# Kernel tuning notes

Hardware: AMD Instinct MI355X
Metric: run time of the kernel (lower is better)

The kernel has to match this reference:

```python
import jax, jax.numpy as jnp
import numpy as np
from jax.scipy.special import logsumexp

B, N, D = 8, 1500, 256
ITERS = 50


def _mlp(x, W1, b1, W2, b2, W3, b3):
    # DETR-style MLP: ReLU between layers, linear last
    h = jax.nn.relu(x @ W1 + b1)
    h = jax.nn.relu(h @ W2 + b2)
    return h @ W3 + b3


def _log_sinkhorn(Z, log_mu, log_nu, iters):
    # Z: [b, m+1, n+1]; loop-carried dual potentials u, v
    u0 = jnp.zeros_like(log_mu)
    v0 = jnp.zeros_like(log_nu)

    def step(carry, _):
        u, v = carry
        u = log_mu - logsumexp(Z + v[:, None, :], axis=2)
        v = log_nu - logsumexp(Z + u[:, :, None], axis=1)
        return (u, v), None

    (u, v), _ = jax.lax.scan(step, (u0, v0), None, length=iters)
    return Z + u[:, :, None] + v[:, None, :]


def _log_optimal_transport(scores, alpha, iters):
    b, m, n = scores.shape
    bins0 = jnp.broadcast_to(alpha, (b, m, 1))
    bins1 = jnp.broadcast_to(alpha, (b, 1, n))
    a = jnp.broadcast_to(alpha, (b, 1, 1))
    couplings = jnp.concatenate(
        [jnp.concatenate([scores, bins0], -1), jnp.concatenate([bins1, a], -1)], 1
    )  # [b, m+1, n+1]
    dt = scores.dtype
    norm = -jnp.log(jnp.asarray(m + n, dt))
    log_mu = jnp.concatenate([jnp.full((m,), norm, dt), jnp.log(jnp.asarray(n, dt))[None] + norm])
    log_nu = jnp.concatenate([jnp.full((n,), norm, dt), jnp.log(jnp.asarray(m, dt))[None] + norm])
    log_mu = jnp.broadcast_to(log_mu[None], (b, m + 1))
    log_nu = jnp.broadcast_to(log_nu[None], (b, n + 1))
    Z = _log_sinkhorn(couplings, log_mu, log_nu, iters)
    return Z - norm


def setup_inputs() -> dict:
    key = jax.random.key(0)
    k = jax.random.split(key, 6)
    s = 0.05
    return {
        "quer_feat": jax.random.normal(k[0], (B, N, D), jnp.float32),
        "pos_start": jax.random.normal(k[1], (B, N, D), jnp.float32),
        "pos_end": jax.random.normal(k[2], (B, N, D), jnp.float32),
        "W1": jax.random.normal(k[3], (2 * D, D), jnp.float32) * s,
        "b1": jnp.zeros((D,), jnp.float32),
        "W2": jax.random.normal(k[4], (D, D), jnp.float32) * s,
        "b2": jnp.zeros((D,), jnp.float32),
        "W3": jax.random.normal(k[5], (D, D), jnp.float32) * s,
        "b3": jnp.zeros((D,), jnp.float32),
        "bin_score": jnp.asarray(1.0, jnp.float32),
        "iters": ITERS,
    }


def reference(quer_feat, pos_start, pos_end, W1, b1, W2, b2, W3, b3, bin_score, iters):
    # forward_single with shared_projection + similarity_based + sinkhorn
    f1 = _mlp(jnp.concatenate([quer_feat, pos_end], -1), W1, b1, W2, b2, W3, b3)
    f2 = _mlp(jnp.concatenate([quer_feat, pos_start], -1), W1, b1, W2, b2, W3, b3)
    scores = jnp.einsum("bnc,bmc->bnm", f1, f2) / jnp.sqrt(jnp.asarray(D, f1.dtype))
    i = jnp.arange(scores.shape[1])
    scores = scores.at[:, i, i].set(-jnp.inf)  # no self-connection
    Z = _log_optimal_transport(scores, bin_score, iters)
    return jnp.exp(Z)
```

## Files before the change

kernel.cpp:

```cpp
#include <hip/hip_runtime.h>
#include <hip/hip_fp16.h>

#define BATCH 8
#define NPTS 1500
#define DIM 256
#define M1 1501
#define KH 1536
#define MROWS 24000
#define ITERS 50
#define MU_PT (1.0f / 3000.0f)
#define MU_BIN 0.5f

typedef _Float16 half8 __attribute__((ext_vector_type(8)));
typedef float f32x4 __attribute__((ext_vector_type(4)));

__device__ __forceinline__ float4 ld4(const float* p){ return *(const float4*)p; }

__global__ void prep_w_kernel(const float* __restrict__ W1, const float* __restrict__ W2,
                              const float* __restrict__ W3, __half* __restrict__ Wt1,
                              __half* __restrict__ Wt2, __half* __restrict__ Wt3)
{
  int gid = blockIdx.x * 256 + threadIdx.x;
  if (gid < 512 * 256) {
    int n = gid >> 9, k = gid & 511;
    Wt1[gid] = __float2half(W1[k * 256 + n]);
  } else if (gid < 512 * 256 + 256 * 256) {
    int g = gid - 512 * 256; int n = g >> 8, k = g & 255;
    Wt2[g] = __float2half(W2[k * 256 + n]);
  } else if (gid < 512 * 256 + 2 * 256 * 256) {
    int g = gid - 512 * 256 - 256 * 256; int n = g >> 8, k = g & 255;
    Wt3[g] = __float2half(W3[k * 256 + n]);
  }
}

template<int MODE>
__global__ __launch_bounds__(256) void mfma_gemm_kernel(
    const float* __restrict__ Aq, const float* __restrict__ Ap_end,
    const float* __restrict__ Ap_start, const __half* __restrict__ Ah,
    const __half* __restrict__ Bh, const float* __restrict__ bias,
    __half* __restrict__ out)
{
  const int K = (MODE == 0) ? 512 : 256;
  const int M = (MODE == 3) ? NPTS : MROWS;
  __shared__ _Float16 As[128][40];
  __shared__ _Float16 Bs[128][40];
  const int t = threadIdx.x;
  const int lane = t & 63;
  const int wave = t >> 6;
  const int quad = lane >> 4, l15 = lane & 15;
  const int wm = wave & 1, wn = wave >> 1;
  const int m0 = blockIdx.x * 128;
  const int n0 = blockIdx.y * 128;
  const int b  = (MODE == 3) ? blockIdx.z : 0;
  const __half* F1 = Ah + (size_t)b * NPTS * 256;
  const __half* F2 = Ah + (size_t)(12000 + b * NPTS) * 256;

  f32x4 acc[4][4];
#pragma unroll
  for (int i = 0; i < 4; ++i)
#pragma unroll
    for (int j = 0; j < 4; ++j) acc[i][j] = (f32x4){0.f, 0.f, 0.f, 0.f};

  const int sr = t >> 1;
  const int c0 = (t & 1) * 16;

  for (int kt = 0; kt < K; kt += 32) {
    {
      int grow = m0 + sr;
      if (MODE == 0) {
        union { half8 v[2]; _Float16 s[16]; } U;
        if (grow < M) {
          int col = kt + c0;
          int r12 = (grow < 12000) ? grow : grow - 12000;
          const float* src;
          if (col < 256) src = Aq + (size_t)r12 * 256 + col;
          else src = ((grow < 12000) ? Ap_end : Ap_start) + (size_t)r12 * 256 + (col - 256);
#pragma unroll
          for (int i = 0; i < 4; ++i) {
            float4 w = ld4(src + 4 * i);
            U.s[4*i+0] = (_Float16)w.x; U.s[4*i+1] = (_Float16)w.y;
            U.s[4*i+2] = (_Float16)w.z; U.s[4*i+3] = (_Float16)w.w;
          }
        } else {
#pragma unroll
          for (int i = 0; i < 16; ++i) U.s[i] = (_Float16)0.f;
        }
        *(half8*)&As[sr][c0]     = U.v[0];
        *(half8*)&As[sr][c0 + 8] = U.v[1];
      } else {
        const __half* src = ((MODE == 3) ? F1 : Ah) + (size_t)grow * 256 + kt + c0;
        uint4 u0 = make_uint4(0,0,0,0), u1 = make_uint4(0,0,0,0);
        if (grow < M) { u0 = *(const uint4*)src; u1 = *(const uint4*)(src + 8); }
        *(uint4*)&As[sr][c0]     = u0;
        *(uint4*)&As[sr][c0 + 8] = u1;
      }
    }
    {
      int n = n0 + sr;
      uint4 u0 = make_uint4(0,0,0,0), u1 = make_uint4(0,0,0,0);
      if (MODE == 3) {
        if (n < NPTS) {
          const __half* src = F2 + (size_t)n * 256 + kt + c0;
          u0 = *(const uint4*)src; u1 = *(const uint4*)(src + 8);
        }
      } else {
        const __half* src = Bh + (size_t)n * K + kt + c0;
        u0 = *(const uint4*)src; u1 = *(const uint4*)(src + 8);
      }
      *(uint4*)&Bs[sr][c0]     = u0;
      *(uint4*)&Bs[sr][c0 + 8] = u1;
    }
    __syncthreads();
    half8 af[4], bf[4];
#pragma unroll
    for (int sm = 0; sm < 4; ++sm)
      af[sm] = *(half8*)&As[wm * 64 + sm * 16 + l15][quad * 8];
#pragma unroll
    for (int sn = 0; sn < 4; ++sn)
      bf[sn] = *(half8*)&Bs[wn * 64 + sn * 16 + l15][quad * 8];
#pragma unroll
    for (int sm = 0; sm < 4; ++sm)
#pragma unroll
      for (int sn = 0; sn < 4; ++sn)
        acc[sm][sn] = __builtin_amdgcn_mfma_f32_16x16x32_f16(af[sm], bf[sn], acc[sm][sn], 0, 0, 0);
    __syncthreads();
  }

  if (MODE == 3) {
    __half* Kb = out + (size_t)b * M1 * KH;
#pragma unroll
    for (int sm = 0; sm < 4; ++sm) {
      int rbase = m0 + wm * 64 + sm * 16 + quad * 4;
#pragma unroll
      for (int reg = 0; reg < 4; ++reg) {
        int gi = rbase + reg;
        if (gi < NPTS) {
#pragma unroll
          for (int sn = 0; sn < 4; ++sn) {
            int gj = n0 + wn * 64 + sn * 16 + l15;
            float v = acc[sm][sn][reg] * 0.0625f;
            float kv = (gj < NPTS && gj != gi) ? __expf(v) : 0.f;
            Kb[(size_t)gi * KH + gj] = __float2half(kv);
          }
        }
      }
    }
  } else {
    float bv[4];
#pragma unroll
    for (int sn = 0; sn < 4; ++sn) bv[sn] = bias[n0 + wn * 64 + sn * 16 + l15];
#pragma unroll
    for (int sm = 0; sm < 4; ++sm) {
      int rbase = m0 + wm * 64 + sm * 16 + quad * 4;
#pragma unroll
      for (int reg = 0; reg < 4; ++reg) {
        int gr = rbase + reg;
        if (gr < MROWS) {
#pragma unroll
          for (int sn = 0; sn < 4; ++sn) {
            int col = n0 + wn * 64 + sn * 16 + l15;
            float v = acc[sm][sn][reg] + bv[sn];
            if (MODE != 2) v = fmaxf(v, 0.f);
            out[(size_t)gr * 256 + col] = __float2half(v);
          }
        }
      }
    }
  }
}

__global__ void bins_kernel(__half* __restrict__ Kh, const float* __restrict__ palpha,
                            float* __restrict__ csum0)
{
  int gid = blockIdx.x * 256 + threadIdx.x;
  if (gid >= BATCH * KH) return;
  int b = gid / KH, x = gid % KH;
  __half He = __float2half(expf(palpha[0]));
  __half* Kb = Kh + (size_t)b * M1 * KH;
  csum0[gid] = 0.f;
  if (x < M1) {
    Kb[(size_t)NPTS * KH + x] = He;
    Kb[(size_t)x * KH + NPTS] = He;
  } else {
    Kb[(size_t)NPTS * KH + x] = __float2half(0.f);
  }
}

__global__ __launch_bounds__(256) void sink_iter_kernel(
    const __half* __restrict__ Kh,
    const float* __restrict__ csum_prev,
    float* __restrict__ csum_cur,
    float* __restrict__ csum_zero,
    float* __restrict__ eu, int first)
{
  const int t = threadIdx.x;
  const int wave = t >> 6, lane = t & 63;
  const int bb = blockIdx.x & 7;
  const int rb = blockIdx.x >> 3;
  const int wv = (rb << 2) | wave;
  const __half* Kb = Kh + (size_t)bb * M1 * KH;
  float* eub = eu + bb * KH;

  __shared__ __align__(16) float evs[KH];
  __shared__ __align__(16) float wpart[4][KH];

  if (rb == 0) {
    for (int j = t; j < KH; j += 256) csum_zero[bb * KH + j] = 0.f;
  }
  if (first) {
    for (int j = t; j < KH; j += 256) evs[j] = (j < M1) ? 1.0f : 0.f;
  } else {
    for (int j = t; j < KH; j += 256) {
      float nu = (j < NPTS) ? MU_PT : ((j == NPTS) ? MU_BIN : 0.f);
      evs[j] = (j < M1) ? (nu / csum_prev[bb * KH + j]) : 0.f;
    }
  }
  __syncthreads();

  float acc[24];
#pragma unroll
  for (int k = 0; k < 24; ++k) acc[k] = 0.f;

  for (int i = wv; i < M1; i += 256) {
    const __half* row = Kb + (size_t)i * KH;
    float r[24];
    float dot = 0.f;
#pragma unroll
    for (int k = 0; k < 3; ++k) {
      int c = lane + (k << 6);
      union { uint4 u; __half2 h[4]; } U;
      U.u = *(const uint4*)(row + (c << 3));
#pragma unroll
      for (int m = 0; m < 4; ++m) {
        float2 f = __half22float2(U.h[m]);
        r[k * 8 + 2 * m]     = f.x;
        r[k * 8 + 2 * m + 1] = f.y;
      }
      float4 e0 = *(const float4*)&evs[(c << 3)];
      float4 e1 = *(const float4*)&evs[(c << 3) + 4];
      dot += r[k*8+0]*e0.x + r[k*8+1]*e0.y + r[k*8+2]*e0.z + r[k*8+3]*e0.w
           + r[k*8+4]*e1.x + r[k*8+5]*e1.y + r[k*8+6]*e1.z + r[k*8+7]*e1.w;
    }
#pragma unroll
    for (int off = 32; off > 0; off >>= 1) dot += __shfl_xor(dot, off);
    float mu = (i < NPTS) ? MU_PT : MU_BIN;
    float euv = mu / dot;
    if (lane == 0) eub[i] = euv;
#pragma unroll
    for (int k = 0; k < 24; ++k) acc[k] += r[k] * euv;
  }

#pragma unroll
  for (int k = 0; k < 3; ++k) {
    int c = lane + (k << 6);
    float4 a0 = make_float4(acc[k*8+0], acc[k*8+1], acc[k*8+2], acc[k*8+3]);
    float4 a1 = make_float4(acc[k*8+4], acc[k*8+5], acc[k*8+6], acc[k*8+7]);
    *(float4*)&wpart[wave][(c << 3)]     = a0;
    *(float4*)&wpart[wave][(c << 3) + 4] = a1;
  }
  __syncthreads();
  for (int j = t; j < M1; j += 256) {
    float s = wpart[0][j] + wpart[1][j] + wpart[2][j] + wpart[3][j];
    atomicAdd(&csum_cur[bb * KH + j], s);
  }
}

__global__ void final_ev_kernel(const float* __restrict__ csum,
                                float* __restrict__ ev)
{
  int j = blockIdx.x * 256 + threadIdx.x;
  int bb = blockIdx.y;
  if (j >= M1) return;
  float nu = (j < NPTS) ? MU_PT : MU_BIN;
  ev[bb * KH + j] = nu / csum[bb * KH + j];
}

__global__ __launch_bounds__(256) void finalize_kernel(
    const __half* __restrict__ Kh, const float* __restrict__ eu,
    const float* __restrict__ ev, float* __restrict__ out)
{
  int rowid = blockIdx.x;
  int b = rowid / M1, i = rowid % M1;
  const __half* krow = Kh + ((size_t)b * M1 + i) * KH;
  const float* evb = ev + b * KH;
  float* orow = out + (size_t)rowid * M1;
  float scale = eu[b * KH + i] * 3000.0f;
  for (int j = threadIdx.x; j < M1; j += 256)
    orow[j] = __half2float(krow[j]) * evb[j] * scale;
}

extern "C" void kernel_launch(void* const* d_in, const int* in_sizes, int n_in,
                              void* d_out, int out_size, void* d_ws, size_t ws_size,
                              hipStream_t stream)
{
  const float* quer      = (const float*)d_in[0];
  const float* pos_start = (const float*)d_in[1];
  const float* pos_end   = (const float*)d_in[2];
  const float* W1 = (const float*)d_in[3];
  const float* b1 = (const float*)d_in[4];
  const float* W2 = (const float*)d_in[5];
  const float* b2 = (const float*)d_in[6];
  const float* W3 = (const float*)d_in[7];
  const float* b3 = (const float*)d_in[8];
  const float* alpha = (const float*)d_in[9];

  char* ws = (char*)d_ws;
  size_t off = 0;
  auto carve = [&](size_t bytes) -> void* {
    void* p = ws + off;
    off += (bytes + 1023) & ~(size_t)1023;
    return p;
  };
  __half* Ha  = (__half*)carve((size_t)MROWS * 256 * 2);
  __half* Hb  = (__half*)carve((size_t)MROWS * 256 * 2);
  __half* Kh  = (__half*)carve((size_t)BATCH * M1 * KH * 2);
  __half* Wt1 = (__half*)carve((size_t)256 * 512 * 2);
  __half* Wt2 = (__half*)carve((size_t)256 * 256 * 2);
  __half* Wt3 = (__half*)carve((size_t)256 * 256 * 2);
  float* csum[3];
  for (int c = 0; c < 3; ++c) csum[c] = (float*)carve((size_t)BATCH * KH * 4);
  float* eu = (float*)carve((size_t)BATCH * KH * 4);
  float* ev = (float*)carve((size_t)BATCH * KH * 4);
  (void)ws_size; (void)in_sizes; (void)n_in; (void)out_size;

  dim3 blk(256);
  prep_w_kernel<<<dim3(1024), blk, 0, stream>>>(W1, W2, W3, Wt1, Wt2, Wt3);
  mfma_gemm_kernel<0><<<dim3(188, 2), blk, 0, stream>>>(quer, pos_end, pos_start, nullptr, Wt1, b1, Ha);
  mfma_gemm_kernel<1><<<dim3(188, 2), blk, 0, stream>>>(nullptr, nullptr, nullptr, Ha, Wt2, b2, Hb);
  mfma_gemm_kernel<2><<<dim3(188, 2), blk, 0, stream>>>(nullptr, nullptr, nullptr, Hb, Wt3, b3, Ha);
  mfma_gemm_kernel<3><<<dim3(12, 12, 8), blk, 0, stream>>>(nullptr, nullptr, nullptr, Ha, nullptr, nullptr, Kh);
  bins_kernel<<<dim3((BATCH * KH + 255) / 256), blk, 0, stream>>>(Kh, alpha, csum[0]);
  for (int it = 0; it < ITERS; ++it) {
    float* prev = csum[(it + 2) % 3];
    float* cur  = csum[it % 3];
    float* znxt = csum[(it + 1) % 3];
    sink_iter_kernel<<<dim3(512), blk, 0, stream>>>(Kh, prev, cur, znxt, eu, it == 0 ? 1 : 0);
  }
  final_ev_kernel<<<dim3(6, 8), blk, 0, stream>>>(csum[(ITERS - 1) % 3], ev);
  finalize_kernel<<<dim3(BATCH * M1), blk, 0, stream>>>(Kh, eu, ev, (float*)d_out);
}
```

Measured before the change: 788.1 us.

## Fuse Sinkhorn iterations into one persistent kernel with register-resident K

Replaces the 50 per-iteration launches with a single persistent kernel of 512 blocks. Each block keeps its rows of the half-precision kernel matrix in registers, so K is loaded from global memory once instead of on every iteration. Blocks synchronize per batch through a global atomic counter barrier, and the finalize step is folded into the same kernel. The risks are a deadlock if all 512 blocks are not co-resident (launch bounds ask for 2 blocks per CU), heavy register pressure, and LDS atomic contention.

```diff
diff --git a/kernel.cpp b/kernel.cpp
--- a/kernel.cpp
+++ b/kernel.cpp
@@ -10,6 +10,7 @@
 #define ITERS 50
 #define MU_PT (1.0f / 3000.0f)
 #define MU_BIN 0.5f
+#define NBB 64
 
 typedef _Float16 half8 __attribute__((ext_vector_type(8)));
 typedef float f32x4 __attribute__((ext_vector_type(4)));
@@ -170,10 +171,11 @@
 }
 
 __global__ void bins_kernel(__half* __restrict__ Kh, const float* __restrict__ palpha,
-                            float* __restrict__ csum0)
+                            float* __restrict__ csum0, unsigned* __restrict__ bar)
 {
   int gid = blockIdx.x * 256 + threadIdx.x;
   if (gid >= BATCH * KH) return;
+  if (gid < BATCH) bar[gid * 64] = 0u;
   int b = gid / KH, x = gid % KH;
   __half He = __float2half(expf(palpha[0]));
   __half* Kb = Kh + (size_t)b * M1 * KH;
@@ -186,107 +188,179 @@
   }
 }
 
-__global__ __launch_bounds__(256) void sink_iter_kernel(
+__global__ __launch_bounds__(256, 2) void sink_fused_kernel(
     const __half* __restrict__ Kh,
-    const float* __restrict__ csum_prev,
-    float* __restrict__ csum_cur,
-    float* __restrict__ csum_zero,
-    float* __restrict__ eu, int first)
+    float* __restrict__ c0, float* __restrict__ c1, float* __restrict__ c2,
+    unsigned* __restrict__ bar, float* __restrict__ out)
 {
   const int t = threadIdx.x;
   const int wave = t >> 6, lane = t & 63;
   const int bb = blockIdx.x & 7;
   const int rb = blockIdx.x >> 3;
-  const int wv = (rb << 2) | wave;
+  const int nrows = (rb < 29) ? 24 : 23;
   const __half* Kb = Kh + (size_t)bb * M1 * KH;
-  float* eub = eu + bb * KH;
-
-  __shared__ __align__(16) float evs[KH];
-  __shared__ __align__(16) float wpart[4][KH];
-
-  if (rb == 0) {
-    for (int j = t; j < KH; j += 256) csum_zero[bb * KH + j] = 0.f;
-  }
-  if (first) {
-    for (int j = t; j < KH; j += 256) evs[j] = (j < M1) ? 1.0f : 0.f;
-  } else {
-    for (int j = t; j < KH; j += 256) {
-      float nu = (j < NPTS) ? MU_PT : ((j == NPTS) ? MU_BIN : 0.f);
-      evs[j] = (j < M1) ? (nu / csum_prev[bb * KH + j]) : 0.f;
-    }
-  }
+  unsigned* mybar = bar + bb * 64;
+
+  __shared__ float cpart[KH];
+
+  uint4 kreg[6][3];
+#pragma unroll
+  for (int q = 0; q < 6; ++q) {
+    int s = wave + (q << 2);
+    if (s < nrows) {
+      const __half* rp = Kb + (size_t)(rb + (s << 6)) * KH + (lane << 3);
+#pragma unroll
+      for (int k = 0; k < 3; ++k) kreg[q][k] = *(const uint4*)(rp + (k << 9));
+    } else {
+#pragma unroll
+      for (int k = 0; k < 3; ++k) kreg[q][k] = make_uint4(0u, 0u, 0u, 0u);
+    }
+  }
+  for (int j = t; j < KH; j += 256) cpart[j] = 0.f;
   __syncthreads();
 
-  float acc[24];
-#pragma unroll
-  for (int k = 0; k < 24; ++k) acc[k] = 0.f;
-
-  for (int i = wv; i < M1; i += 256) {
-    const __half* row = Kb + (size_t)i * KH;
-    float r[24];
-    float dot = 0.f;
+  float* cprev = c2;
+  float* ccur  = c0;
+  float* cnext = c1;
+
+  float ev[24];
+  float euk[6];
+
+  for (int it = 0; it < ITERS; ++it) {
+    if (it == 0) {
+#pragma unroll
+      for (int k = 0; k < 3; ++k) {
+        int cbase = (lane << 3) + (k << 9);
+#pragma unroll
+        for (int j = 0; j < 8; ++j) ev[k * 8 + j] = (cbase + j < M1) ? 1.0f : 0.f;
+      }
+    } else {
+      const float* cp = cprev + bb * KH;
+#pragma unroll
+      for (int k = 0; k < 3; ++k) {
+        int cbase = (lane << 3) + (k << 9);
+        float4 a = *(const float4*)(cp + cbase);
+        float4 bq = *(const float4*)(cp + cbase + 4);
+        float cs[8] = {a.x, a.y, a.z, a.w, bq.x, bq.y, bq.z, bq.w};
+#pragma unroll
+        for (int j = 0; j < 8; ++j) {
+          int col = cbase + j;
+          float nu = (col < NPTS) ? MU_PT : ((col == NPTS) ? MU_BIN : 0.f);
+          ev[k * 8 + j] = (col < M1) ? (nu / cs[j]) : 0.f;
+        }
+      }
+    }
+    if (t < 24) cnext[bb * KH + rb * 24 + t] = 0.f;
+
+    float acc[24];
+#pragma unroll
+    for (int j = 0; j < 24; ++j) acc[j] = 0.f;
+#pragma unroll
+    for (int q = 0; q < 6; ++q) {
+      int s = wave + (q << 2);
+      if (s < nrows) {
+        int row = rb + (s << 6);
+        float r[24], dot = 0.f;
+#pragma unroll
+        for (int k = 0; k < 3; ++k) {
+          union { uint4 u; __half2 h[4]; } U;
+          U.u = kreg[q][k];
+#pragma unroll
+          for (int m = 0; m < 4; ++m) {
+            float2 f = __half22float2(U.h[m]);
+            r[k * 8 + 2 * m]     = f.x;
+            r[k * 8 + 2 * m + 1] = f.y;
+          }
+          dot += r[k*8+0]*ev[k*8+0] + r[k*8+1]*ev[k*8+1] + r[k*8+2]*ev[k*8+2] + r[k*8+3]*ev[k*8+3]
+               + r[k*8+4]*ev[k*8+4] + r[k*8+5]*ev[k*8+5] + r[k*8+6]*ev[k*8+6] + r[k*8+7]*ev[k*8+7];
+        }
+#pragma unroll
+        for (int off = 32; off > 0; off >>= 1) dot += __shfl_xor(dot, off);
+        float mu = (row < NPTS) ? MU_PT : MU_BIN;
+        float euv = mu / dot;
+        euk[q] = euv;
+#pragma unroll
+        for (int j = 0; j < 24; ++j) acc[j] += r[j] * euv;
+      }
+    }
+
+#pragma unroll
+    for (int k = 0; k < 3; ++k)
+#pragma unroll
+      for (int j = 0; j < 8; ++j)
+        atomicAdd(&cpart[(((k << 3) + j) << 6) + lane], acc[k * 8 + j]);
+    __syncthreads();
+
+    {
+      float* cc = ccur + bb * KH;
+#pragma unroll
+      for (int p = 0; p < 6; ++p) {
+        int c = t + (p << 8);
+        int kk = c >> 9, rem = c & 511;
+        int idx = (((kk << 3) + (rem & 7)) << 6) + (rem >> 3);
+        float v = cpart[idx];
+        cpart[idx] = 0.f;
+        if (c < M1) atomicAdd(&cc[c], v);
+      }
+    }
+
+    __syncthreads();
+    if (t == 0) {
+      __threadfence();
+      atomicAdd(mybar, 1u);
+      unsigned tgt = (unsigned)NBB * (unsigned)(it + 1);
+      while (__hip_atomic_load(mybar, __ATOMIC_RELAXED, __HIP_MEMORY_SCOPE_AGENT) < tgt)
+        __builtin_amdgcn_s_sleep(2);
+      __threadfence();
+    }
+    __syncthreads();
+
+    float* tmp = cprev; cprev = ccur; ccur = cnext; cnext = tmp;
+  }
+
+  float evf[24];
+  {
+    const float* cp = cprev + bb * KH;
 #pragma unroll
     for (int k = 0; k < 3; ++k) {
-      int c = lane + (k << 6);
-      union { uint4 u; __half2 h[4]; } U;
-      U.u = *(const uint4*)(row + (c << 3));
-#pragma unroll
-      for (int m = 0; m < 4; ++m) {
-        float2 f = __half22float2(U.h[m]);
-        r[k * 8 + 2 * m]     = f.x;
-        r[k * 8 + 2 * m + 1] = f.y;
-      }
-      float4 e0 = *(const float4*)&evs[(c << 3)];
-      float4 e1 = *(const float4*)&evs[(c << 3) + 4];
-      dot += r[k*8+0]*e0.x + r[k*8+1]*e0.y + r[k*8+2]*e0.z + r[k*8+3]*e0.w
-           + r[k*8+4]*e1.x + r[k*8+5]*e1.y + r[k*8+6]*e1.z + r[k*8+7]*e1.w;
-    }
-#pragma unroll
-    for (int off = 32; off > 0; off >>= 1) dot += __shfl_xor(dot, off);
-    float mu = (i < NPTS) ? MU_PT : MU_BIN;
-    float euv = mu / dot;
-    if (lane == 0) eub[i] = euv;
-#pragma unroll
-    for (int k = 0; k < 24; ++k) acc[k] += r[k] * euv;
-  }
-
-#pragma unroll
-  for (int k = 0; k < 3; ++k) {
-    int c = lane + (k << 6);
-    float4 a0 = make_float4(acc[k*8+0], acc[k*8+1], acc[k*8+2], acc[k*8+3]);
-    float4 a1 = make_float4(acc[k*8+4], acc[k*8+5], acc[k*8+6], acc[k*8+7]);
-    *(float4*)&wpart[wave][(c << 3)]     = a0;
-    *(float4*)&wpart[wave][(c << 3) + 4] = a1;
-  }
-  __syncthreads();
-  for (int j = t; j < M1; j += 256) {
-    float s = wpart[0][j] + wpart[1][j] + wpart[2][j] + wpart[3][j];
-    atomicAdd(&csum_cur[bb * KH + j], s);
-  }
-}
-
-__global__ void final_ev_kernel(const float* __restrict__ csum,
-                                float* __restrict__ ev)
-{
-  int j = blockIdx.x * 256 + threadIdx.x;
-  int bb = blockIdx.y;
-  if (j >= M1) return;
-  float nu = (j < NPTS) ? MU_PT : MU_BIN;
-  ev[bb * KH + j] = nu / csum[bb * KH + j];
-}
-
-__global__ __launch_bounds__(256) void finalize_kernel(
-    const __half* __restrict__ Kh, const float* __restrict__ eu,
-    const float* __restrict__ ev, float* __restrict__ out)
-{
-  int rowid = blockIdx.x;
-  int b = rowid / M1, i = rowid % M1;
-  const __half* krow = Kh + ((size_t)b * M1 + i) * KH;
-  const float* evb = ev + b * KH;
-  float* orow = out + (size_t)rowid * M1;
-  float scale = eu[b * KH + i] * 3000.0f;
-  for (int j = threadIdx.x; j < M1; j += 256)
-    orow[j] = __half2float(krow[j]) * evb[j] * scale;
+      int cbase = (lane << 3) + (k << 9);
+      float4 a = *(const float4*)(cp + cbase);
+      float4 bq = *(const float4*)(cp + cbase + 4);
+      float cs[8] = {a.x, a.y, a.z, a.w, bq.x, bq.y, bq.z, bq.w};
+#pragma unroll
+      for (int j = 0; j < 8; ++j) {
+        int col = cbase + j;
+        float nu = (col < NPTS) ? MU_PT : ((col == NPTS) ? MU_BIN : 0.f);
+        evf[k * 8 + j] = (col < M1) ? (nu / cs[j]) : 0.f;
+      }
+    }
+  }
+#pragma unroll
+  for (int q = 0; q < 6; ++q) {
+    int s = wave + (q << 2);
+    if (s < nrows) {
+      int row = rb + (s << 6);
+      float scale = euk[q] * 3000.0f;
+      float* orow = out + ((size_t)bb * M1 + row) * M1;
+#pragma unroll
+      for (int k = 0; k < 3; ++k) {
+        union { uint4 u; __half2 h[4]; } U;
+        U.u = kreg[q][k];
+        float f[8];
+#pragma unroll
+        for (int m = 0; m < 4; ++m) {
+          float2 g = __half22float2(U.h[m]);
+          f[2 * m] = g.x; f[2 * m + 1] = g.y;
+        }
+        int cb = (lane << 3) + (k << 9);
+#pragma unroll
+        for (int j = 0; j < 8; ++j) {
+          int col = cb + j;
+          if (col < M1) orow[col] = f[j] * evf[k * 8 + j] * scale;
+        }
+      }
+    }
+  }
 }
 
 extern "C" void kernel_launch(void* const* d_in, const int* in_sizes, int n_in,
@@ -319,8 +393,7 @@
   __half* Wt3 = (__half*)carve((size_t)256 * 256 * 2);
   float* csum[3];
   for (int c = 0; c < 3; ++c) csum[c] = (float*)carve((size_t)BATCH * KH * 4);
-  float* eu = (float*)carve((size_t)BATCH * KH * 4);
-  float* ev = (float*)carve((size_t)BATCH * KH * 4);
+  unsigned* bar = (unsigned*)carve((size_t)BATCH * 64 * sizeof(unsigned));
   (void)ws_size; (void)in_sizes; (void)n_in; (void)out_size;
 
   dim3 blk(256);
@@ -329,13 +402,6 @@
   mfma_gemm_kernel<1><<<dim3(188, 2), blk, 0, stream>>>(nullptr, nullptr, nullptr, Ha, Wt2, b2, Hb);
   mfma_gemm_kernel<2><<<dim3(188, 2), blk, 0, stream>>>(nullptr, nullptr, nullptr, Hb, Wt3, b3, Ha);
   mfma_gemm_kernel<3><<<dim3(12, 12, 8), blk, 0, stream>>>(nullptr, nullptr, nullptr, Ha, nullptr, nullptr, Kh);
-  bins_kernel<<<dim3((BATCH * KH + 255) / 256), blk, 0, stream>>>(Kh, alpha, csum[0]);
-  for (int it = 0; it < ITERS; ++it) {
-    float* prev = csum[(it + 2) % 3];
-    float* cur  = csum[it % 3];
-    float* znxt = csum[(it + 1) % 3];
-    sink_iter_kernel<<<dim3(512), blk, 0, stream>>>(Kh, prev, cur, znxt, eu, it == 0 ? 1 : 0);
-  }
-  final_ev_kernel<<<dim3(6, 8), blk, 0, stream>>>(csum[(ITERS - 1) % 3], ev);
-  finalize_kernel<<<dim3(BATCH * M1), blk, 0, stream>>>(Kh, eu, ev, (float*)d_out);
+  bins_kernel<<<dim3((BATCH * KH + 255) / 256), blk, 0, stream>>>(Kh, alpha, csum[0], bar);
+  sink_fused_kernel<<<dim3(512), blk, 0, stream>>>(Kh, csum[0], csum[1], csum[2], bar, (float*)d_out);
 }
```

Result: slower. 2.427 ms (+207.9%).
